# Performance work log

Hardware: AMD Instinct MI355X
Metric: run time of the kernel (lower is better)

## Reference

```python
import jax, jax.numpy as jnp
import numpy as np

EPS = 1e-6


def setup_inputs() -> dict:
    key = jax.random.key(0)
    k1, k2, k3, k4 = jax.random.split(key, 4)
    B, N, D = 8, 4096, 512
    x = jax.random.normal(k1, (B, N, D), dtype=jnp.float32)
    # torch nn.Linear(dim, 3*dim, bias=False): weight shape [3D, D], y = x @ W.T
    w_qkv = jax.random.normal(k2, (3 * D, D), dtype=jnp.float32) * (1.0 / np.sqrt(D))
    w_proj = jax.random.normal(k3, (D, D), dtype=jnp.float32) * (1.0 / np.sqrt(D))
    b_proj = jax.random.normal(k4, (D,), dtype=jnp.float32) * 0.01
    return {"x": x, "w_qkv": w_qkv, "w_proj": w_proj, "b_proj": b_proj, "heads": 8}


def reference(x, w_qkv, w_proj, b_proj, heads):
    B, N, D = x.shape
    H = heads
    d = D // H
    # qkv projection -> (3, B, H, N, d)
    qkv = (x @ w_qkv.T).reshape(B, N, 3, H, d).transpose(2, 0, 3, 1, 4)
    q, k, v = qkv[0], qkv[1], qkv[2]
    # elu+1 feature map (positive features)
    q = jax.nn.elu(q) + 1.0 + EPS
    k = jax.nn.elu(k) + 1.0 + EPS
    # kv summary: [B,H,d,d]
    kv = jnp.einsum('bhnd,bhne->bhde', k, v)
    # denominator: q . sum_n(k) -> [B,H,N]
    denom = jnp.einsum('bhnd,bhd->bhn', q, k.sum(axis=2))
    out = jnp.einsum('bhnd,bhde->bhne', q, kv) / (denom[..., None] + EPS)
    out = out.transpose(0, 2, 1, 3).reshape(B, N, D)
    return out @ w_proj.T + b_proj
```

## Files before the change

kernel.cpp:

```cpp
#include <hip/hip_runtime.h>
#include <hip/hip_bf16.h>
#include <math.h>

#define EPSF 1e-6f

constexpr int Bc = 8;
constexpr int Nc = 4096;
constexpr int Dc = 512;
constexpr int QKVC = 3 * Dc;

typedef __attribute__((ext_vector_type(8))) short short8v;
typedef __attribute__((ext_vector_type(8))) unsigned short ushort8v;
typedef __attribute__((ext_vector_type(4))) float float4v;

__device__ __forceinline__ unsigned short f2bf(float f) {
    union { float f; unsigned int u; } v; v.f = f;
    unsigned int u = v.u;
    return (unsigned short)((u + 0x7fffu + ((u >> 16) & 1u)) >> 16);
}
__device__ __forceinline__ float bf2f(unsigned short h) {
    union { unsigned int u; float f; } v; v.u = ((unsigned int)h) << 16;
    return v.f;
}

typedef __attribute__((address_space(1))) const void gvoid_t;
typedef __attribute__((address_space(3))) void lvoid_t;
__device__ __forceinline__ void llds16(const void* g, void* l) {
    __builtin_amdgcn_global_load_lds((gvoid_t*)g, (lvoid_t*)l, 16, 0, 0);
}

__global__ __launch_bounds__(256) void cvt_f32_bf16(
    const float* __restrict__ in, unsigned short* __restrict__ out, int n8)
{
    int i = blockIdx.x * 256 + threadIdx.x;
    if (i >= n8) return;
    float4 a = reinterpret_cast<const float4*>(in)[2 * i];
    float4 b = reinterpret_cast<const float4*>(in)[2 * i + 1];
    ushort8v o;
    o[0] = f2bf(a.x); o[1] = f2bf(a.y); o[2] = f2bf(a.z); o[3] = f2bf(a.w);
    o[4] = f2bf(b.x); o[5] = f2bf(b.y); o[6] = f2bf(b.z); o[7] = f2bf(b.w);
    reinterpret_cast<ushort8v*>(out)[i] = o;
}

__global__ __launch_bounds__(512, 2) void gemm_qkv(
    const unsigned short* __restrict__ A,
    const unsigned short* __restrict__ Bm,
    unsigned short* __restrict__ Cout)
{
    constexpr int LDA = 512, LDB = 512, LDC = 1536;
    constexpr int NT = 8;
    __shared__ unsigned short ring[3][24576];

    const int t = threadIdx.x;
    const int orig = blockIdx.x;
    const int wg = (orig & 7) * 192 + (orig >> 3);
    const int bm = (wg / 12) * 256;
    const int bn = (wg % 12) * 128;

    const int w = t >> 6, lane = t & 63;
    const int ln = lane & 15, g = lane >> 4;
    const int wr = (w >> 1) * 64;
    const int wc = (w & 1) * 64;
    const int l7 = ln & 7;

    const int rs = t >> 3;
    const int ci = t & 7;
    const int swz = ci ^ (rs & 7);
    const unsigned short* As0 = A + (size_t)(bm + rs) * LDA + swz * 8;
    const unsigned short* As1 = A + (size_t)(bm + 64 + rs) * LDA + swz * 8;
    const unsigned short* As2 = A + (size_t)(bm + 128 + rs) * LDA + swz * 8;
    const unsigned short* As3 = A + (size_t)(bm + 192 + rs) * LDA + swz * 8;
    const unsigned short* Bs0 = Bm + (size_t)(bn + rs) * LDB + swz * 8;
    const unsigned short* Bs1 = Bm + (size_t)(bn + 64 + rs) * LDB + swz * 8;

#define STAGEQ(Tt) do {                                                        \
        const int k0_ = (Tt) * 64;                                             \
        unsigned short* dA_ = &ring[(Tt) % 3][0];                              \
        unsigned short* dB_ = &ring[(Tt) % 3][16384];                          \
        llds16(As0 + k0_, dA_ + (size_t)t * 8);                                \
        llds16(As1 + k0_, dA_ + (size_t)(512 + t) * 8);                        \
        llds16(As2 + k0_, dA_ + (size_t)(1024 + t) * 8);                       \
        llds16(As3 + k0_, dA_ + (size_t)(1536 + t) * 8);                       \
        llds16(Bs0 + k0_, dB_ + (size_t)t * 8);                                \
        llds16(Bs1 + k0_, dB_ + (size_t)(512 + t) * 8);                        \
    } while (0)

    float4v acc[4][4];
#pragma unroll
    for (int i = 0; i < 4; ++i)
#pragma unroll
        for (int j = 0; j < 4; ++j) acc[i][j] = {0.f, 0.f, 0.f, 0.f};

    STAGEQ(0);
    STAGEQ(1);
    asm volatile("s_waitcnt vmcnt(6)" ::: "memory");
    __builtin_amdgcn_s_barrier();
    __builtin_amdgcn_sched_barrier(0);

#pragma unroll
    for (int T = 0; T < NT; ++T) {
        if (T + 2 < NT) STAGEQ(T + 2);

        const unsigned short* base = &ring[T % 3][0];
        short8v a[4][2], b[4][2];
#pragma unroll
        for (int i = 0; i < 4; ++i)
#pragma unroll
            for (int kk = 0; kk < 2; ++kk) {
                const int row = wr + i * 16 + ln;
                a[i][kk] = *reinterpret_cast<const short8v*>(
                    base + row * 64 + (((kk * 4 + g) ^ l7) << 3));
            }
#pragma unroll
        for (int j = 0; j < 4; ++j)
#pragma unroll
            for (int kk = 0; kk < 2; ++kk) {
                const int row = wc + j * 16 + ln;
                b[j][kk] = *reinterpret_cast<const short8v*>(
                    base + 16384 + row * 64 + (((kk * 4 + g) ^ l7) << 3));
            }

        __builtin_amdgcn_s_setprio(1);
#pragma unroll
        for (int kk = 0; kk < 2; ++kk)
#pragma unroll
            for (int i = 0; i < 4; ++i)
#pragma unroll
                for (int j = 0; j < 4; ++j)
                    acc[i][j] = __builtin_amdgcn_mfma_f32_16x16x32_bf16(
                        a[i][kk], b[j][kk], acc[i][j], 0, 0, 0);
        __builtin_amdgcn_s_setprio(0);

        if (T + 1 < NT) {
            if (T + 2 < NT)
                asm volatile("s_waitcnt vmcnt(6)" ::: "memory");
            else
                asm volatile("s_waitcnt vmcnt(0)" ::: "memory");
            __builtin_amdgcn_s_barrier();
            __builtin_amdgcn_sched_barrier(0);
        }
    }
#undef STAGEQ

#pragma unroll
    for (int i = 0; i < 4; ++i) {
        const int Rb = bm + wr + i * 16 + g * 4;
#pragma unroll
        for (int j = 0; j < 4; ++j) {
            const int Cc = bn + wc + j * 16 + ln;
            const bool do_elu = (Cc < 1024);
#pragma unroll
            for (int r = 0; r < 4; ++r) {
                float v = acc[i][j][r];
                if (do_elu) v = (v > 0.f) ? (v + 1.0f + EPSF) : (expf(v) + EPSF);
                Cout[(size_t)(Rb + r) * LDC + Cc] = f2bf(v);
            }
        }
    }
}

__global__ __launch_bounds__(256) void kv_part(
    const unsigned short* __restrict__ qkv,
    float* __restrict__ kvp, float* __restrict__ ksp)
{
    const int bh = blockIdx.x, chunk = blockIdx.y;
    const int b = bh >> 3, h = bh & 7;

    __shared__ float kt[64][68];
    __shared__ float vt[64][68];
    __shared__ float ksl[4][64];

    const int t  = threadIdx.x;
    const int e  = t & 63, dg = t >> 6;
    const int rr = t >> 3, slot = t & 7;

    float acc[16] = {};
    float ks = 0.f;

    const size_t base = ((size_t)b * Nc + (size_t)chunk * 512) * QKVC + h * 64;

    for (int n0 = 0; n0 < 512; n0 += 64) {
#pragma unroll
        for (int half = 0; half < 2; ++half) {
            const int row = rr + half * 32;
            const unsigned short* kr = qkv + base + (size_t)(n0 + row) * QKVC + Dc + slot * 8;
            const unsigned short* vr = kr + Dc;
            ushort8v kq = *reinterpret_cast<const ushort8v*>(kr);
            ushort8v vq = *reinterpret_cast<const ushort8v*>(vr);
            float4 k0 = make_float4(bf2f(kq[0]), bf2f(kq[1]), bf2f(kq[2]), bf2f(kq[3]));
            float4 k1 = make_float4(bf2f(kq[4]), bf2f(kq[5]), bf2f(kq[6]), bf2f(kq[7]));
            float4 v0 = make_float4(bf2f(vq[0]), bf2f(vq[1]), bf2f(vq[2]), bf2f(vq[3]));
            float4 v1 = make_float4(bf2f(vq[4]), bf2f(vq[5]), bf2f(vq[6]), bf2f(vq[7]));
            *reinterpret_cast<float4*>(&kt[row][slot * 8])     = k0;
            *reinterpret_cast<float4*>(&kt[row][slot * 8 + 4]) = k1;
            *reinterpret_cast<float4*>(&vt[row][slot * 8])     = v0;
            *reinterpret_cast<float4*>(&vt[row][slot * 8 + 4]) = v1;
        }
        __syncthreads();
#pragma unroll 2
        for (int nn = 0; nn < 64; ++nn) {
            const float vv = vt[nn][e];
            const float4 q0 = *reinterpret_cast<const float4*>(&kt[nn][dg * 16]);
            const float4 q1 = *reinterpret_cast<const float4*>(&kt[nn][dg * 16 + 4]);
            const float4 q2 = *reinterpret_cast<const float4*>(&kt[nn][dg * 16 + 8]);
            const float4 q3 = *reinterpret_cast<const float4*>(&kt[nn][dg * 16 + 12]);
            acc[0]  += q0.x * vv; acc[1]  += q0.y * vv; acc[2]  += q0.z * vv; acc[3]  += q0.w * vv;
            acc[4]  += q1.x * vv; acc[5]  += q1.y * vv; acc[6]  += q1.z * vv; acc[7]  += q1.w * vv;
            acc[8]  += q2.x * vv; acc[9]  += q2.y * vv; acc[10] += q2.z * vv; acc[11] += q2.w * vv;
            acc[12] += q3.x * vv; acc[13] += q3.y * vv; acc[14] += q3.z * vv; acc[15] += q3.w * vv;
        }
#pragma unroll
        for (int nn = 0; nn < 16; ++nn) ks += kt[dg * 16 + nn][e];
        __syncthreads();
    }

    float* kvpp = kvp + ((size_t)bh * 8 + chunk) * 4096;
#pragma unroll
    for (int i = 0; i < 16; ++i) kvpp[(dg * 16 + i) * 64 + e] = acc[i];

    ksl[dg][e] = ks;
    __syncthreads();
    if (t < 64) ksp[((size_t)bh * 8 + chunk) * 64 + t] =
        ksl[0][t] + ksl[1][t] + ksl[2][t] + ksl[3][t];
}

__global__ __launch_bounds__(256) void kv_reduce(
    const float* __restrict__ kvp, const float* __restrict__ ksp,
    unsigned short* __restrict__ kvb, float* __restrict__ ksum)
{
    const int bh = blockIdx.x, t = threadIdx.x;
    const float* src = kvp + (size_t)bh * 8 * 4096;
#pragma unroll
    for (int i = 0; i < 16; ++i) {
        const int idx = i * 256 + t;
        float s = 0.f;
#pragma unroll
        for (int c = 0; c < 8; ++c) s += src[c * 4096 + idx];
        kvb[(size_t)bh * 4096 + idx] = f2bf(s);
    }
    if (t < 64) {
        float s = 0.f;
#pragma unroll
        for (int c = 0; c < 8; ++c) s += ksp[((size_t)bh * 8 + c) * 64 + t];
        ksum[bh * 64 + t] = s;
    }
}

__global__ __launch_bounds__(256) void gemm_M(
    const unsigned short* __restrict__ kvb,
    const unsigned short* __restrict__ wp,
    unsigned short* __restrict__ MT)
{
    const int bh = blockIdx.x, b = bh >> 3, h = bh & 7;
    const int t = threadIdx.x, w = t >> 6, lane = t & 63;
    const int ln = lane & 15, g = lane >> 4;

    float4v acc[8][4];
#pragma unroll
    for (int i = 0; i < 8; ++i)
#pragma unroll
        for (int j = 0; j < 4; ++j) acc[i][j] = {0.f, 0.f, 0.f, 0.f};

#pragma unroll
    for (int kk = 0; kk < 2; ++kk) {
        short8v a[8], bf[4];
#pragma unroll
        for (int i = 0; i < 8; ++i)
            a[i] = *reinterpret_cast<const short8v*>(
                wp + (size_t)(w * 128 + i * 16 + ln) * 512 + h * 64 + kk * 32 + g * 8);
#pragma unroll
        for (int j = 0; j < 4; ++j)
            bf[j] = *reinterpret_cast<const short8v*>(
                kvb + (size_t)bh * 4096 + (j * 16 + ln) * 64 + kk * 32 + g * 8);
#pragma unroll
        for (int i = 0; i < 8; ++i)
#pragma unroll
            for (int j = 0; j < 4; ++j)
                acc[i][j] = __builtin_amdgcn_mfma_f32_16x16x32_bf16(a[i], bf[j], acc[i][j], 0, 0, 0);
    }

#pragma unroll
    for (int i = 0; i < 8; ++i) {
        const int c0 = w * 128 + i * 16 + g * 4;
#pragma unroll
        for (int j = 0; j < 4; ++j) {
            const int d = j * 16 + ln;
#pragma unroll
            for (int r = 0; r < 4; ++r)
                MT[(size_t)b * 262144 + (size_t)(c0 + r) * 512 + h * 64 + d] =
                    f2bf(acc[i][j][r]);
        }
    }
}

__global__ __launch_bounds__(256) void q_scale(
    unsigned short* __restrict__ qkv, const float* __restrict__ ksum)
{
    __shared__ float kss[512];
    const int blk = blockIdx.x;
    const int b = blk >> 7;
    const int t = threadIdx.x;
    kss[t] = ksum[b * 512 + t];
    kss[t + 256] = ksum[b * 512 + 256 + t];
    __syncthreads();

    const int row = blk * 32 + (t >> 3);
    const int h = t & 7;
    unsigned short* p = qkv + (size_t)row * QKVC + h * 64;

    ushort8v v[8];
#pragma unroll
    for (int s = 0; s < 8; ++s) v[s] = *reinterpret_cast<const ushort8v*>(p + s * 8);

    float den = EPSF;
#pragma unroll
    for (int s = 0; s < 8; ++s)
#pragma unroll
        for (int m = 0; m < 8; ++m)
            den += bf2f(v[s][m]) * kss[h * 64 + s * 8 + m];
    const float inv = 1.0f / den;

#pragma unroll
    for (int s = 0; s < 8; ++s) {
        ushort8v o;
#pragma unroll
        for (int m = 0; m < 8; ++m) o[m] = f2bf(bf2f(v[s][m]) * inv);
        *reinterpret_cast<ushort8v*>(p + s * 8) = o;
    }
}

__global__ __launch_bounds__(512, 2) void gemm_out(
    const unsigned short* __restrict__ A,
    const unsigned short* __restrict__ Bt,
    const float* __restrict__ bias,
    float* __restrict__ out)
{
    constexpr int LDA = 1536, LDB = 512, NT = 8;
    __shared__ unsigned short ring[3][24576];

    const int t = threadIdx.x;
    const int orig = blockIdx.x;
    const int wg = (orig & 7) * 64 + (orig >> 3);
    const int bm = (wg >> 2) * 256;
    const int bn = (wg & 3) * 128;
    const unsigned short* Bm = Bt + (size_t)(bm >> 12) * 262144;

    const int w = t >> 6, lane = t & 63;
    const int ln = lane & 15, g = lane >> 4;
    const int wr = (w >> 1) * 64;
    const int wc = (w & 1) * 64;
    const int l7 = ln & 7;

    const int rs = t >> 3;
    const int ci = t & 7;
    const int swz = ci ^ (rs & 7);
    const unsigned short* As0 = A + (size_t)(bm + rs) * LDA + swz * 8;
    const unsigned short* As1 = A + (size_t)(bm + 64 + rs) * LDA + swz * 8;
    const unsigned short* As2 = A + (size_t)(bm + 128 + rs) * LDA + swz * 8;
    const unsigned short* As3 = A + (size_t)(bm + 192 + rs) * LDA + swz * 8;
    const unsigned short* Bs0 = Bm + (size_t)(bn + rs) * LDB + swz * 8;
    const unsigned short* Bs1 = Bm + (size_t)(bn + 64 + rs) * LDB + swz * 8;

#define STAGEO(Tt) do {                                                        \
        const int k0_ = (Tt) * 64;                                             \
        unsigned short* dA_ = &ring[(Tt) % 3][0];                              \
        unsigned short* dB_ = &ring[(Tt) % 3][16384];                          \
        llds16(As0 + k0_, dA_ + (size_t)t * 8);                                \
        llds16(As1 + k0_, dA_ + (size_t)(512 + t) * 8);                        \
        llds16(As2 + k0_, dA_ + (size_t)(1024 + t) * 8);                       \
        llds16(As3 + k0_, dA_ + (size_t)(1536 + t) * 8);                       \
        llds16(Bs0 + k0_, dB_ + (size_t)t * 8);                                \
        llds16(Bs1 + k0_, dB_ + (size_t)(512 + t) * 8);                        \
    } while (0)

    float4v acc[4][4];
#pragma unroll
    for (int i = 0; i < 4; ++i)
#pragma unroll
        for (int j = 0; j < 4; ++j) acc[i][j] = {0.f, 0.f, 0.f, 0.f};

    STAGEO(0);
    STAGEO(1);
    asm volatile("s_waitcnt vmcnt(6)" ::: "memory");
    __builtin_amdgcn_s_barrier();
    __builtin_amdgcn_sched_barrier(0);

#pragma unroll
    for (int T = 0; T < NT; ++T) {
        if (T + 2 < NT) STAGEO(T + 2);

        const unsigned short* base = &ring[T % 3][0];
        short8v a[4][2], b[4][2];
#pragma unroll
        for (int i = 0; i < 4; ++i)
#pragma unroll
            for (int kk = 0; kk < 2; ++kk) {
                const int row = wr + i * 16 + ln;
                a[i][kk] = *reinterpret_cast<const short8v*>(
                    base + row * 64 + (((kk * 4 + g) ^ l7) << 3));
            }
#pragma unroll
        for (int j = 0; j < 4; ++j)
#pragma unroll
            for (int kk = 0; kk < 2; ++kk) {
                const int row = wc + j * 16 + ln;
                b[j][kk] = *reinterpret_cast<const short8v*>(
                    base + 16384 + row * 64 + (((kk * 4 + g) ^ l7) << 3));
            }

        __builtin_amdgcn_s_setprio(1);
#pragma unroll
        for (int kk = 0; kk < 2; ++kk)
#pragma unroll
            for (int i = 0; i < 4; ++i)
#pragma unroll
                for (int j = 0; j < 4; ++j)
                    acc[i][j] = __builtin_amdgcn_mfma_f32_16x16x32_bf16(
                        a[i][kk], b[j][kk], acc[i][j], 0, 0, 0);
        __builtin_amdgcn_s_setprio(0);

        if (T + 1 < NT) {
            if (T + 2 < NT)
                asm volatile("s_waitcnt vmcnt(6)" ::: "memory");
            else
                asm volatile("s_waitcnt vmcnt(0)" ::: "memory");
            __builtin_amdgcn_s_barrier();
            __builtin_amdgcn_sched_barrier(0);
        }
    }
#undef STAGEO

#pragma unroll
    for (int i = 0; i < 4; ++i) {
        const int Rb = bm + wr + i * 16 + g * 4;
#pragma unroll
        for (int j = 0; j < 4; ++j) {
            const int Cc = bn + wc + j * 16 + ln;
            const float bv = bias[Cc];
#pragma unroll
            for (int r = 0; r < 4; ++r)
                out[(size_t)(Rb + r) * 512 + Cc] = acc[i][j][r] + bv;
        }
    }
}

extern "C" void kernel_launch(void* const* d_in, const int* in_sizes, int n_in,
                              void* d_out, int out_size, void* d_ws, size_t ws_size,
                              hipStream_t stream)
{
    const float* x      = (const float*)d_in[0];
    const float* w_qkv  = (const float*)d_in[1];
    const float* w_proj = (const float*)d_in[2];
    const float* b_proj = (const float*)d_in[3];
    float* out = (float*)d_out;

    char* ws = (char*)d_ws;
    unsigned short* qkvb = (unsigned short*)ws;
    size_t off = (size_t)32768 * 1536 * 2;
    unsigned short* xb   = (unsigned short*)(ws + off); off += (size_t)32768 * 512 * 2;
    unsigned short* wqb  = (unsigned short*)(ws + off); off += (size_t)1536 * 512 * 2;
    unsigned short* wpb  = (unsigned short*)(ws + off); off += (size_t)512 * 512 * 2;
    float* kvp           = (float*)(ws + off);          off += (size_t)64 * 8 * 4096 * 4;
    float* ksp           = (float*)(ws + off);          off += (size_t)64 * 8 * 64 * 4;
    unsigned short* kvb  = (unsigned short*)(ws + off); off += (size_t)64 * 4096 * 2;
    float* ksumb         = (float*)(ws + off);          off += (size_t)64 * 64 * 4;
    unsigned short* MT   = (unsigned short*)(ws + off); off += (size_t)8 * 512 * 512 * 2;

    cvt_f32_bf16<<<dim3((32768 * 512 / 8 + 255) / 256), dim3(256), 0, stream>>>(x, xb, 32768 * 512 / 8);
    cvt_f32_bf16<<<dim3((1536 * 512 / 8 + 255) / 256), dim3(256), 0, stream>>>(w_qkv, wqb, 1536 * 512 / 8);
    cvt_f32_bf16<<<dim3((512 * 512 / 8 + 255) / 256), dim3(256), 0, stream>>>(w_proj, wpb, 512 * 512 / 8);

    gemm_qkv<<<dim3(1536), dim3(512), 0, stream>>>(xb, wqb, qkvb);

    kv_part<<<dim3(64, 8), dim3(256), 0, stream>>>(qkvb, kvp, ksp);
    kv_reduce<<<dim3(64), dim3(256), 0, stream>>>(kvp, ksp, kvb, ksumb);

    gemm_M<<<dim3(64), dim3(256), 0, stream>>>(kvb, wpb, MT);

    q_scale<<<dim3(1024), dim3(256), 0, stream>>>(qkvb, ksumb);

    gemm_out<<<dim3(512), dim3(512), 0, stream>>>(qkvb, MT, b_proj, out);
}
```

Before: 192.5 us.

## Retile kv_part with transposed swizzled LDS and 4x4 register blocking; merge weight casts

Rewrites the per-chunk K^T V accumulation so each thread computes a 4x4 register tile from K and V stored transposed in LDS with an XOR swizzle. Each thread now reads float4 vectors along n instead of broadcast rows, which raises FMA work per LDS load. The K column sums are now accumulated during the staging load, and the partial sums are reduced across 16 slots. The two weight-conversion launches are merged into one kernel to save a launch. This adds register pressure and swizzle index arithmetic.

Result: slower. 199.0 us (+3.4%).

```diff
diff --git a/kernel.cpp b/kernel.cpp
--- a/kernel.cpp
+++ b/kernel.cpp
@@ -40,6 +40,23 @@
     o[0] = f2bf(a.x); o[1] = f2bf(a.y); o[2] = f2bf(a.z); o[3] = f2bf(a.w);
     o[4] = f2bf(b.x); o[5] = f2bf(b.y); o[6] = f2bf(b.z); o[7] = f2bf(b.w);
     reinterpret_cast<ushort8v*>(out)[i] = o;
+}
+
+__global__ __launch_bounds__(256) void cvt_weights(
+    const float* __restrict__ wq, const float* __restrict__ wp,
+    unsigned short* __restrict__ wqo, unsigned short* __restrict__ wpo)
+{
+    const int i = blockIdx.x * 256 + threadIdx.x;
+    const int NQ = 1536 * 512 / 8;
+    const float* src; unsigned short* dst; int idx;
+    if (i < NQ) { src = wq; dst = wqo; idx = i; }
+    else        { src = wp; dst = wpo; idx = i - NQ; }
+    float4 a = reinterpret_cast<const float4*>(src)[2 * idx];
+    float4 b = reinterpret_cast<const float4*>(src)[2 * idx + 1];
+    ushort8v o;
+    o[0] = f2bf(a.x); o[1] = f2bf(a.y); o[2] = f2bf(a.z); o[3] = f2bf(a.w);
+    o[4] = f2bf(b.x); o[5] = f2bf(b.y); o[6] = f2bf(b.z); o[7] = f2bf(b.w);
+    reinterpret_cast<ushort8v*>(dst)[idx] = o;
 }
 
 __global__ __launch_bounds__(512, 2) void gemm_qkv(
@@ -166,62 +183,83 @@
     const int bh = blockIdx.x, chunk = blockIdx.y;
     const int b = bh >> 3, h = bh & 7;
 
-    __shared__ float kt[64][68];
-    __shared__ float vt[64][68];
-    __shared__ float ksl[4][64];
-
-    const int t  = threadIdx.x;
-    const int e  = t & 63, dg = t >> 6;
-    const int rr = t >> 3, slot = t & 7;
-
-    float acc[16] = {};
-    float ks = 0.f;
-
-    const size_t base = ((size_t)b * Nc + (size_t)chunk * 512) * QKVC + h * 64;
-
-    for (int n0 = 0; n0 < 512; n0 += 64) {
-#pragma unroll
-        for (int half = 0; half < 2; ++half) {
-            const int row = rr + half * 32;
-            const unsigned short* kr = qkv + base + (size_t)(n0 + row) * QKVC + Dc + slot * 8;
-            const unsigned short* vr = kr + Dc;
-            ushort8v kq = *reinterpret_cast<const ushort8v*>(kr);
-            ushort8v vq = *reinterpret_cast<const ushort8v*>(vr);
-            float4 k0 = make_float4(bf2f(kq[0]), bf2f(kq[1]), bf2f(kq[2]), bf2f(kq[3]));
-            float4 k1 = make_float4(bf2f(kq[4]), bf2f(kq[5]), bf2f(kq[6]), bf2f(kq[7]));
-            float4 v0 = make_float4(bf2f(vq[0]), bf2f(vq[1]), bf2f(vq[2]), bf2f(vq[3]));
-            float4 v1 = make_float4(bf2f(vq[4]), bf2f(vq[5]), bf2f(vq[6]), bf2f(vq[7]));
-            *reinterpret_cast<float4*>(&kt[row][slot * 8])     = k0;
-            *reinterpret_cast<float4*>(&kt[row][slot * 8 + 4]) = k1;
-            *reinterpret_cast<float4*>(&vt[row][slot * 8])     = v0;
-            *reinterpret_cast<float4*>(&vt[row][slot * 8 + 4]) = v1;
+    __shared__ float ktT[4096];
+    __shared__ float vtT[4096];
+    __shared__ float ksl[16][64];
+
+    const int t = threadIdx.x;
+    const int di = t >> 4, ej = t & 15;
+    const bool isK = (t < 128);
+    const int ts = isK ? t : t - 128;
+    const int slot = ts & 7;
+    const int ng = ts >> 3;
+
+    const size_t base = ((size_t)b * Nc + (size_t)chunk * 512) * QKVC + h * 64
+                      + (isK ? Dc : 2 * Dc) + slot * 8;
+
+    float acc[4][4] = {};
+    float ks8[8] = {};
+
+    for (int it = 0; it < 8; ++it) {
+        {
+            const unsigned short* src = qkv + base + (size_t)(it * 64 + 4 * ng) * QKVC;
+            ushort8v r0 = *reinterpret_cast<const ushort8v*>(src);
+            ushort8v r1 = *reinterpret_cast<const ushort8v*>(src + QKVC);
+            ushort8v r2 = *reinterpret_cast<const ushort8v*>(src + 2 * QKVC);
+            ushort8v r3 = *reinterpret_cast<const ushort8v*>(src + 3 * QKVC);
+            float* dst = isK ? ktT : vtT;
+#pragma unroll
+            for (int i = 0; i < 8; ++i) {
+                const int row = 8 * slot + i;
+                float4 wv = make_float4(bf2f(r0[i]), bf2f(r1[i]), bf2f(r2[i]), bf2f(r3[i]));
+                *reinterpret_cast<float4*>(dst + row * 64 + ((ng ^ (row & 15)) << 2)) = wv;
+                if (isK) ks8[i] += wv.x + wv.y + wv.z + wv.w;
+            }
         }
         __syncthreads();
-#pragma unroll 2
-        for (int nn = 0; nn < 64; ++nn) {
-            const float vv = vt[nn][e];
-            const float4 q0 = *reinterpret_cast<const float4*>(&kt[nn][dg * 16]);
-            const float4 q1 = *reinterpret_cast<const float4*>(&kt[nn][dg * 16 + 4]);
-            const float4 q2 = *reinterpret_cast<const float4*>(&kt[nn][dg * 16 + 8]);
-            const float4 q3 = *reinterpret_cast<const float4*>(&kt[nn][dg * 16 + 12]);
-            acc[0]  += q0.x * vv; acc[1]  += q0.y * vv; acc[2]  += q0.z * vv; acc[3]  += q0.w * vv;
-            acc[4]  += q1.x * vv; acc[5]  += q1.y * vv; acc[6]  += q1.z * vv; acc[7]  += q1.w * vv;
-            acc[8]  += q2.x * vv; acc[9]  += q2.y * vv; acc[10] += q2.z * vv; acc[11] += q2.w * vv;
-            acc[12] += q3.x * vv; acc[13] += q3.y * vv; acc[14] += q3.z * vv; acc[15] += q3.w * vv;
-        }
-#pragma unroll
-        for (int nn = 0; nn < 16; ++nn) ks += kt[dg * 16 + nn][e];
+
+#pragma unroll 4
+        for (int nc = 0; nc < 16; ++nc) {
+            float4 kd[4], ve[4];
+#pragma unroll
+            for (int i = 0; i < 4; ++i)
+                kd[i] = *reinterpret_cast<const float4*>(
+                    ktT + (di + 16 * i) * 64 + ((nc ^ di) << 2));
+#pragma unroll
+            for (int j = 0; j < 4; ++j)
+                ve[j] = *reinterpret_cast<const float4*>(
+                    vtT + (ej + 16 * j) * 64 + ((nc ^ ej) << 2));
+#pragma unroll
+            for (int i = 0; i < 4; ++i)
+#pragma unroll
+                for (int j = 0; j < 4; ++j) {
+                    acc[i][j] += kd[i].x * ve[j].x;
+                    acc[i][j] += kd[i].y * ve[j].y;
+                    acc[i][j] += kd[i].z * ve[j].z;
+                    acc[i][j] += kd[i].w * ve[j].w;
+                }
+        }
         __syncthreads();
     }
 
     float* kvpp = kvp + ((size_t)bh * 8 + chunk) * 4096;
 #pragma unroll
-    for (int i = 0; i < 16; ++i) kvpp[(dg * 16 + i) * 64 + e] = acc[i];
-
-    ksl[dg][e] = ks;
+    for (int i = 0; i < 4; ++i)
+#pragma unroll
+        for (int j = 0; j < 4; ++j)
+            kvpp[(di + 16 * i) * 64 + (ej + 16 * j)] = acc[i][j];
+
+    if (isK) {
+#pragma unroll
+        for (int i = 0; i < 8; ++i) ksl[ng][8 * slot + i] = ks8[i];
+    }
     __syncthreads();
-    if (t < 64) ksp[((size_t)bh * 8 + chunk) * 64 + t] =
-        ksl[0][t] + ksl[1][t] + ksl[2][t] + ksl[3][t];
+    if (t < 64) {
+        float s = 0.f;
+#pragma unroll
+        for (int c = 0; c < 16; ++c) s += ksl[c][t];
+        ksp[((size_t)bh * 8 + chunk) * 64 + t] = s;
+    }
 }
 
 __global__ __launch_bounds__(256) void kv_reduce(
@@ -467,8 +505,8 @@
     unsigned short* MT   = (unsigned short*)(ws + off); off += (size_t)8 * 512 * 512 * 2;
 
     cvt_f32_bf16<<<dim3((32768 * 512 / 8 + 255) / 256), dim3(256), 0, stream>>>(x, xb, 32768 * 512 / 8);
-    cvt_f32_bf16<<<dim3((1536 * 512 / 8 + 255) / 256), dim3(256), 0, stream>>>(w_qkv, wqb, 1536 * 512 / 8);
-    cvt_f32_bf16<<<dim3((512 * 512 / 8 + 255) / 256), dim3(256), 0, stream>>>(w_proj, wpb, 512 * 512 / 8);
+    cvt_weights<<<dim3(((1536 * 512 + 512 * 512) / 8 + 255) / 256), dim3(256), 0, stream>>>(
+        w_qkv, w_proj, wqb, wpb);
 
     gemm_qkv<<<dim3(1536), dim3(512), 0, stream>>>(xb, wqb, qkvb);
 
```
